# Optimization experiments

Hardware: AMD Instinct MI355X
Metric: run time of the kernel (lower is better)

Reference implementation:

```python
import jax, jax.numpy as jnp
import numpy as np

N = 50000
E = 1600000
IN_FEATS = 256
HIDDEN = 32
HEADS = 4
NUM_CLASSES = 16
NEG_SLOPE = 0.2  # DGL GATConv default leaky_relu slope


def gat_conv(x, src, dst, W, b, attn_l, attn_r, n_nodes):
    """DGL-style GATConv. x:[N,Fin], W:[Fin,H*D], attn_l/attn_r:[H,D], b:[H*D].
    Returns [N, H, D]."""
    H, D = attn_l.shape
    feat = (x @ W).reshape(-1, H, D)                     # [N,H,D]
    el = jnp.sum(feat * attn_l, axis=-1)                 # [N,H]
    er = jnp.sum(feat * attn_r, axis=-1)                 # [N,H]
    e = jax.nn.leaky_relu(el[src] + er[dst], NEG_SLOPE)  # [E,H]
    # segment softmax over incoming edges of each dst node
    m = jax.ops.segment_max(e, dst, num_segments=n_nodes)
    m = jnp.where(jnp.isfinite(m), m, 0.0)               # empty segments -> -inf
    ex = jnp.exp(e - m[dst])                             # [E,H]
    denom = jax.ops.segment_sum(ex, dst, num_segments=n_nodes)
    alpha = ex / jnp.maximum(denom, 1e-9)[dst]           # [E,H]
    msg = feat[src] * alpha[:, :, None]                  # [E,H,D]
    out = jax.ops.segment_sum(msg, dst, num_segments=n_nodes)
    return out + b.reshape(H, D)


def setup_inputs() -> dict:
    key = jax.random.key(0)
    ks = jax.random.split(key, 12)
    x = jax.random.normal(ks[0], (N, IN_FEATS), dtype=jnp.float32)
    src = jax.random.randint(ks[1], (E,), 0, N, dtype=jnp.int32)
    dst = jax.random.randint(ks[2], (E,), 0, N, dtype=jnp.int32)
    s1 = 1.0 / np.sqrt(IN_FEATS)
    W1 = jax.random.normal(ks[3], (IN_FEATS, HEADS * HIDDEN), dtype=jnp.float32) * s1
    b1 = jnp.zeros((HEADS * HIDDEN,), dtype=jnp.float32)
    al1 = jax.random.normal(ks[4], (HEADS, HIDDEN), dtype=jnp.float32) * 0.1
    ar1 = jax.random.normal(ks[5], (HEADS, HIDDEN), dtype=jnp.float32) * 0.1
    F2 = HEADS * HIDDEN
    s2 = 1.0 / np.sqrt(F2)
    W2 = jax.random.normal(ks[6], (F2, NUM_CLASSES), dtype=jnp.float32) * s2
    b2 = jnp.zeros((NUM_CLASSES,), dtype=jnp.float32)
    al2 = jax.random.normal(ks[7], (1, NUM_CLASSES), dtype=jnp.float32) * 0.1
    ar2 = jax.random.normal(ks[8], (1, NUM_CLASSES), dtype=jnp.float32) * 0.1
    return {"x": x, "src": src, "dst": dst,
            "W1": W1, "b1": b1, "al1": al1, "ar1": ar1,
            "W2": W2, "b2": b2, "al2": al2, "ar2": ar2}


def reference(x, src, dst, W1, b1, al1, ar1, W2, b2, al2, ar2):
    h = jax.nn.elu(gat_conv(x, src, dst, W1, b1, al1, ar1, N))  # [N,H,D]
    h = h.reshape(N, HEADS * HIDDEN)                            # flatten(1)
    out = gat_conv(h, src, dst, W2, b2, al2, ar2, N)            # [N,1,C]
    return out.mean(axis=1)                                     # [N,C]
```

## Files before the change

kernel.cpp:

```cpp
#include <hip/hip_runtime.h>
#include <hip/hip_fp16.h>

#define N_NODES 50000
#define N_EDGES 1600000
#define FIN 256
#define HD 128
#define NHEADS 4
#define C2 16
#define NEG 0.2f

#define EBLK 4096
#define NBLK 391
#define NBUCK 391
#define BSH 7
#define BMASK 127
#define MAXB 5120

typedef _Float16 v8h __attribute__((ext_vector_type(8)));
typedef float v4f __attribute__((ext_vector_type(4)));
union F4H8 { float4 f; v8h h; };

__device__ __forceinline__ float elu1(float x) { return x > 0.f ? x : __expf(x) - 1.f; }
__device__ __forceinline__ float lexp(float e) { return __expf(e > 0.f ? e : NEG * e); }


__global__ __launch_bounds__(256) void k_bhist(const int* __restrict__ dst,
                                               int* __restrict__ ghist) {
    __shared__ int lh[NBUCK];
    int tid = threadIdx.x, b = blockIdx.x;
    for (int t = tid; t < NBUCK; t += 256) lh[t] = 0;
    __syncthreads();
    int base = b * EBLK;
    int nq = (min(EBLK, N_EDGES - base)) >> 2;
    const int4* d4 = (const int4*)(dst + base);
    for (int q = tid; q < nq; q += 256) {
        int4 d = d4[q];
        atomicAdd(&lh[d.x >> BSH], 1);
        atomicAdd(&lh[d.y >> BSH], 1);
        atomicAdd(&lh[d.z >> BSH], 1);
        atomicAdd(&lh[d.w >> BSH], 1);
    }
    __syncthreads();
    for (int t = tid; t < NBUCK; t += 256) ghist[t * NBLK + b] = lh[t];
}

__global__ __launch_bounds__(256) void k_bscan1(int* __restrict__ ghist,
                                                int* __restrict__ bucket_tot) {
    __shared__ int s[256];
    int B = blockIdx.x, t = threadIdx.x;
    int* row = ghist + (size_t)B * NBLK;
    int i0 = 2 * t, i1 = 2 * t + 1;
    int a0 = (i0 < NBLK) ? row[i0] : 0;
    int a1 = (i1 < NBLK) ? row[i1] : 0;
    int pair = a0 + a1;
    s[t] = pair;
    __syncthreads();
    for (int off = 1; off < 256; off <<= 1) {
        int u = (t >= off) ? s[t - off] : 0;
        __syncthreads();
        s[t] += u;
        __syncthreads();
    }
    int excl = s[t] - pair;
    if (i0 < NBLK) row[i0] = excl;
    if (i1 < NBLK) row[i1] = excl + a0;
    if (t == 255) bucket_tot[B] = s[255];
}

__global__ __launch_bounds__(512) void k_bscan2(const int* __restrict__ bucket_tot,
                                                int* __restrict__ bucket_base,
                                                int* __restrict__ rowstart) {
    __shared__ int s[512];
    int t = threadIdx.x;
    int v = (t < NBUCK) ? bucket_tot[t] : 0;
    s[t] = v;
    __syncthreads();
    for (int off = 1; off < 512; off <<= 1) {
        int u = (t >= off) ? s[t - off] : 0;
        __syncthreads();
        s[t] += u;
        __syncthreads();
    }
    if (t < NBUCK) bucket_base[t] = s[t] - v;
    if (t == 0) { bucket_base[NBUCK] = N_EDGES; rowstart[N_NODES] = N_EDGES; }
}

__global__ __launch_bounds__(256) void k_bscatter(
        const int* __restrict__ src, const int* __restrict__ dst,
        const int* __restrict__ ghist, const int* __restrict__ bucket_base,
        int* __restrict__ ebuf) {
    __shared__ int lcur[NBUCK];
    int tid = threadIdx.x, b = blockIdx.x;
    for (int t = tid; t < NBUCK; t += 256)
        lcur[t] = bucket_base[t] + ghist[t * NBLK + b];
    __syncthreads();
    int base = b * EBLK;
    int nq = (min(EBLK, N_EDGES - base)) >> 2;
    const int4* s4 = (const int4*)(src + base);
    const int4* d4 = (const int4*)(dst + base);
    for (int q = tid; q < nq; q += 256) {
        int4 s = s4[q];
        int4 d = d4[q];
        int p;
        p = atomicAdd(&lcur[d.x >> BSH], 1); ebuf[p] = (s.x << BSH) | (d.x & BMASK);
        p = atomicAdd(&lcur[d.y >> BSH], 1); ebuf[p] = (s.y << BSH) | (d.y & BMASK);
        p = atomicAdd(&lcur[d.z >> BSH], 1); ebuf[p] = (s.z << BSH) | (d.z & BMASK);
        p = atomicAdd(&lcur[d.w >> BSH], 1); ebuf[p] = (s.w << BSH) | (d.w & BMASK);
    }
}

__global__ __launch_bounds__(256) void k_bsort(
        const int* __restrict__ ebuf, const int* __restrict__ bucket_base,
        int* __restrict__ sorted_src, int* __restrict__ rowstart) {
    __shared__ int ein[MAXB];
    __shared__ int eout[MAXB];
    __shared__ int hist[128];
    __shared__ int sc[128];
    __shared__ int cursor[128];
    int tid = threadIdx.x, B = blockIdx.x;
    int base = bucket_base[B];
    int n = bucket_base[B + 1] - base;
    if (tid < 128) hist[tid] = 0;
    __syncthreads();
    for (int i = tid; i < n; i += 256) {
        int v = ebuf[base + i];
        ein[i] = v;
        atomicAdd(&hist[v & BMASK], 1);
    }
    __syncthreads();
    if (tid < 128) sc[tid] = hist[tid];
    __syncthreads();
    for (int off = 1; off < 128; off <<= 1) {
        int u = 0;
        if (tid < 128 && tid >= off) u = sc[tid - off];
        __syncthreads();
        if (tid < 128) sc[tid] += u;
        __syncthreads();
    }
    if (tid < 128) {
        int ex = sc[tid] - hist[tid];
        cursor[tid] = ex;
        int node = B * 128 + tid;
        if (node < N_NODES) rowstart[node] = base + ex;
    }
    __syncthreads();
    for (int i = tid; i < n; i += 256) {
        int v = ein[i];
        int p = atomicAdd(&cursor[v & BMASK], 1);
        eout[p] = v >> BSH;
    }
    __syncthreads();
    for (int i = tid; i < n; i += 256) sorted_src[base + i] = eout[i];
}


__global__ __launch_bounds__(256) void k_w1half(const float* __restrict__ W1,
                                                _Float16* __restrict__ W1T) {
    int idx = blockIdx.x * 256 + threadIdx.x;
    int k = idx >> 7, c = idx & 127;
    W1T[c * 256 + k] = (_Float16)W1[idx];
}


__global__ __launch_bounds__(256) void k_gemm1(
        const float* __restrict__ x, const _Float16* __restrict__ W1T,
        const float* __restrict__ al1, const float* __restrict__ ar1,
        __half* __restrict__ feat1h, float* __restrict__ el1, float* __restrict__ er1) {
    __shared__ v8h As[64 * 4];
    __shared__ v8h Bs[128 * 4];
    int tid = threadIdx.x;
    int nb = blockIdx.x * 64;
    int wid = tid >> 6, lane = tid & 63;
    int wm = wid & 1, wn = wid >> 1;
    int q = lane >> 4, lm = lane & 15;

    int anode = tid >> 2, ach = tid & 3;
    int gnode = nb + anode; if (gnode >= N_NODES) gnode = N_NODES - 1;
    const float4* xrow = (const float4*)(x + (size_t)gnode * FIN);
    int bc = tid >> 2, bch = tid & 3;

    v4f acc[2][4];
    #pragma unroll
    for (int mt = 0; mt < 2; mt++)
        #pragma unroll
        for (int nt = 0; nt < 4; nt++) acc[mt][nt] = (v4f)(0.f);

    float4 xa0 = xrow[ach * 2];
    float4 xa1 = xrow[ach * 2 + 1];
    F4H8 wb0, wb1;
    wb0.f = *(const float4*)(W1T + bc * 256 + bch * 8);
    wb1.f = *(const float4*)(W1T + (bc + 64) * 256 + bch * 8);

    for (int step = 0; step < 8; step++) {
        __syncthreads();
        {
            v8h av;
            av[0] = (_Float16)xa0.x; av[1] = (_Float16)xa0.y;
            av[2] = (_Float16)xa0.z; av[3] = (_Float16)xa0.w;
            av[4] = (_Float16)xa1.x; av[5] = (_Float16)xa1.y;
            av[6] = (_Float16)xa1.z; av[7] = (_Float16)xa1.w;
            As[anode * 4 + (ach ^ (anode & 3))] = av;
            Bs[bc * 4 + (bch ^ (bc & 3))] = wb0.h;
            Bs[(bc + 64) * 4 + (bch ^ (bc & 3))] = wb1.h;
        }
        __syncthreads();
        if (step < 7) {
            int k0 = (step + 1) * 32;
            xa0 = xrow[(k0 >> 2) + ach * 2];
            xa1 = xrow[(k0 >> 2) + ach * 2 + 1];
            wb0.f = *(const float4*)(W1T + bc * 256 + k0 + bch * 8);
            wb1.f = *(const float4*)(W1T + (bc + 64) * 256 + k0 + bch * 8);
        }
        v8h af[2], bf[4];
        #pragma unroll
        for (int mt = 0; mt < 2; mt++) {
            int nl = wm * 32 + mt * 16 + lm;
            af[mt] = As[nl * 4 + (q ^ (nl & 3))];
        }
        #pragma unroll
        for (int nt = 0; nt < 4; nt++) {
            int cl = wn * 64 + nt * 16 + lm;
            bf[nt] = Bs[cl * 4 + (q ^ (cl & 3))];
        }
        #pragma unroll
        for (int mt = 0; mt < 2; mt++)
            #pragma unroll
            for (int nt = 0; nt < 4; nt++)
                acc[mt][nt] = __builtin_amdgcn_mfma_f32_16x16x32_f16(
                    af[mt], bf[nt], acc[mt][nt], 0, 0, 0);
    }

    float alv[4], arv[4];
    #pragma unroll
    for (int nt = 0; nt < 4; nt++) {
        alv[nt] = al1[wn * 64 + nt * 16 + lm];
        arv[nt] = ar1[wn * 64 + nt * 16 + lm];
    }
    int h0 = 2 * wn, h1 = 2 * wn + 1;
    #pragma unroll
    for (int mt = 0; mt < 2; mt++) {
        #pragma unroll
        for (int r = 0; r < 4; r++) {
            int node = nb + wm * 32 + mt * 16 + q * 4 + r;
            bool ok = node < N_NODES;
            float v0 = acc[mt][0][r], v1 = acc[mt][1][r];
            float v2 = acc[mt][2][r], v3 = acc[mt][3][r];
            if (ok) {
                __half* fp = feat1h + (size_t)node * HD + wn * 64 + lm;
                fp[0]  = __float2half(v0);
                fp[16] = __float2half(v1);
                fp[32] = __float2half(v2);
                fp[48] = __float2half(v3);
            }
            float pl0 = v0 * alv[0] + v1 * alv[1];
            float pr0 = v0 * arv[0] + v1 * arv[1];
            float pl1 = v2 * alv[2] + v3 * alv[3];
            float pr1 = v2 * arv[2] + v3 * arv[3];
            #pragma unroll
            for (int m = 1; m <= 8; m <<= 1) {
                pl0 += __shfl_xor(pl0, m); pr0 += __shfl_xor(pr0, m);
                pl1 += __shfl_xor(pl1, m); pr1 += __shfl_xor(pr1, m);
            }
            if (ok && lm == 0) {
                el1[node * 4 + h0] = pl0; er1[node * 4 + h0] = pr0;
                el1[node * 4 + h1] = pl1; er1[node * 4 + h1] = pr1;
            }
        }
    }
}


__global__ __launch_bounds__(256) void k_agg1(
        const int* __restrict__ rowstart, const int* __restrict__ sorted_src,
        const float* __restrict__ el1, const float* __restrict__ er1,
        const __half* __restrict__ feat1h, const float* __restrict__ b1,
        float* __restrict__ h) {
    int tid = threadIdx.x;
    int d = blockIdx.x * 4 + (tid >> 6);
    int lane = tid & 63;
    int eg = lane >> 4;
    int cl = lane & 15;
    int head = cl >> 2;
    float er = er1[d * 4 + head];
    int start = rowstart[d], end = rowstart[d + 1];
    float acc[8];
    #pragma unroll
    for (int k = 0; k < 8; k++) acc[k] = 0.f;
    float wsum = 0.f;

    for (int i = start; i < end; i += 16) {
        int s[4]; bool ok[4];
        #pragma unroll
        for (int u = 0; u < 4; u++) {
            int e = i + 4 * u + eg;
            ok[u] = e < end;
            int ec = ok[u] ? e : end - 1;
            s[u] = sorted_src[ec];
        }
        float elv[4];
        #pragma unroll
        for (int u = 0; u < 4; u++) elv[u] = el1[s[u] * 4 + head];
        F4H8 r[4];
        #pragma unroll
        for (int u = 0; u < 4; u++)
            r[u].f = *(const float4*)(feat1h + (size_t)s[u] * HD + cl * 8);
        #pragma unroll
        for (int u = 0; u < 4; u++) {
            float w = ok[u] ? lexp(elv[u] + er) : 0.f;
            #pragma unroll
            for (int k = 0; k < 8; k++)
                acc[k] = fmaf((float)r[u].h[k], w, acc[k]);
            wsum += w;
        }
    }
    #pragma unroll
    for (int k = 0; k < 8; k++) {
        acc[k] += __shfl_xor(acc[k], 16);
        acc[k] += __shfl_xor(acc[k], 32);
    }
    wsum += __shfl_xor(wsum, 16);
    wsum += __shfl_xor(wsum, 32);
    if (eg == 0) {
        float inv = 1.f / fmaxf(wsum, 1e-9f);
        float v[8];
        #pragma unroll
        for (int k = 0; k < 8; k++) v[k] = elu1(acc[k] * inv + b1[cl * 8 + k]);
        float4* hp = (float4*)(h + (size_t)d * HD + cl * 8);
        hp[0] = make_float4(v[0], v[1], v[2], v[3]);
        hp[1] = make_float4(v[4], v[5], v[6], v[7]);
    }
}


__global__ __launch_bounds__(256) void k_gemm2(
        const float* __restrict__ h, const float* __restrict__ W2,
        const float* __restrict__ al2, const float* __restrict__ ar2,
        float* __restrict__ feat2, float* __restrict__ el2, float* __restrict__ er2) {
    __shared__ float hs[16 * 132];
    __shared__ float w2t[16 * 132];
    int tid = threadIdx.x;
    int nb = blockIdx.x * 16;
    for (int idx = tid; idx < 512; idx += 256) {
        int row = idx >> 5, kk = idx & 31;
        ((float4*)(hs + row * 132))[kk] = ((const float4*)h)[(size_t)(nb + row) * 32 + kk];
    }
    for (int idx = tid; idx < 2048; idx += 256) {
        int k = idx >> 4, c = idx & 15;
        w2t[c * 132 + k] = W2[idx];
    }
    __syncthreads();
    int nl = tid >> 4, col = tid & 15;
    const float4* hv = (const float4*)(hs + nl * 132);
    const float4* wv = (const float4*)(w2t + col * 132);
    float acc = 0.f;
    #pragma unroll
    for (int kk = 0; kk < 32; kk++) {
        float4 a = hv[kk], w = wv[kk];
        acc += a.x * w.x + a.y * w.y + a.z * w.z + a.w * w.w;
    }
    int node = nb + nl;
    feat2[node * 16 + col] = acc;
    float pl = acc * al2[col], pr = acc * ar2[col];
    #pragma unroll
    for (int m = 8; m >= 1; m >>= 1) {
        pl += __shfl_xor(pl, m);
        pr += __shfl_xor(pr, m);
    }
    if (col == 0) { el2[node] = pl; er2[node] = pr; }
}


__global__ __launch_bounds__(256) void k_agg2(
        const int* __restrict__ rowstart, const int* __restrict__ sorted_src,
        const float* __restrict__ el2, const float* __restrict__ er2,
        const float* __restrict__ feat2, const float* __restrict__ b2,
        float* __restrict__ out) {
    int tid = threadIdx.x;
    int d = blockIdx.x * 4 + (tid >> 6);
    int lane = tid & 63;
    int eg = lane >> 2;
    int cq = lane & 3;
    float er = er2[d];
    int start = rowstart[d], end = rowstart[d + 1];
    float4 acc = make_float4(0.f, 0.f, 0.f, 0.f);
    float wsum = 0.f;
    for (int i = start; i < end; i += 16) {
        int e = i + eg;
        bool ok = e < end;
        int ec = ok ? e : end - 1;
        int s = sorted_src[ec];
        float elv = el2[s];
        float4 f = ((const float4*)feat2)[(size_t)s * 4 + cq];
        float ev = elv + er;
        float wr = __expf(ev > 0.f ? ev : NEG * ev);
        float w = ok ? wr : 0.f;
        acc.x += w * f.x; acc.y += w * f.y; acc.z += w * f.z; acc.w += w * f.w;
        wsum += w;
    }
    #pragma unroll
    for (int m = 4; m <= 32; m <<= 1) {
        acc.x += __shfl_xor(acc.x, m);
        acc.y += __shfl_xor(acc.y, m);
        acc.z += __shfl_xor(acc.z, m);
        acc.w += __shfl_xor(acc.w, m);
        wsum  += __shfl_xor(wsum, m);
    }
    if (lane < 4) {
        float inv = 1.f / fmaxf(wsum, 1e-9f);
        float4 bv = ((const float4*)b2)[cq];
        float4 o = make_float4(acc.x * inv + bv.x, acc.y * inv + bv.y,
                               acc.z * inv + bv.z, acc.w * inv + bv.w);
        ((float4*)out)[(size_t)d * 4 + cq] = o;
    }
}


extern "C" void kernel_launch(void* const* d_in, const int* in_sizes, int n_in,
                              void* d_out, int out_size, void* d_ws, size_t ws_size,
                              hipStream_t stream) {
    const float* x   = (const float*)d_in[0];
    const int*   src = (const int*)d_in[1];
    const int*   dst = (const int*)d_in[2];
    const float* W1  = (const float*)d_in[3];
    const float* b1  = (const float*)d_in[4];
    const float* al1 = (const float*)d_in[5];
    const float* ar1 = (const float*)d_in[6];
    const float* W2  = (const float*)d_in[7];
    const float* b2  = (const float*)d_in[8];
    const float* al2 = (const float*)d_in[9];
    const float* ar2 = (const float*)d_in[10];
    float* out = (float*)d_out;

    char* ws = (char*)d_ws;
    size_t off = 0;
    auto alloc = [&](size_t bytes) -> char* {
        char* p = ws + off;
        off += (bytes + 255) & ~(size_t)255;
        return p;
    };
    __half* feat1h     = (__half*)alloc((size_t)N_NODES * HD * 2);
    _Float16* W1T      = (_Float16*)alloc((size_t)FIN * HD * 2);
    float* h           = (float*)alloc((size_t)N_NODES * HD * 4);
    float* el1         = (float*)alloc((size_t)N_NODES * 4 * 4);
    float* er1         = (float*)alloc((size_t)N_NODES * 4 * 4);
    float* feat2       = (float*)alloc((size_t)N_NODES * C2 * 4);
    float* el2         = (float*)alloc((size_t)N_NODES * 4);
    float* er2         = (float*)alloc((size_t)N_NODES * 4);
    int*   ghist       = (int*)alloc((size_t)NBUCK * NBLK * 4);
    int*   bucket_tot  = (int*)alloc((size_t)NBUCK * 4);
    int*   bucket_base = (int*)alloc((size_t)(NBUCK + 1) * 4);
    int*   rowstart    = (int*)alloc((size_t)(N_NODES + 1) * 4);
    int*   ebuf        = (int*)alloc((size_t)N_EDGES * 4);
    int*   sorted_src  = (int*)alloc((size_t)N_EDGES * 4);

    k_bhist<<<NBLK, 256, 0, stream>>>(dst, ghist);
    k_bscan1<<<NBUCK, 256, 0, stream>>>(ghist, bucket_tot);
    k_bscan2<<<1, 512, 0, stream>>>(bucket_tot, bucket_base, rowstart);
    k_bscatter<<<NBLK, 256, 0, stream>>>(src, dst, ghist, bucket_base, ebuf);
    k_bsort<<<NBUCK, 256, 0, stream>>>(ebuf, bucket_base, sorted_src, rowstart);
    k_w1half<<<128, 256, 0, stream>>>(W1, W1T);
    k_gemm1<<<(N_NODES + 63) / 64, 256, 0, stream>>>(x, W1T, al1, ar1, feat1h, el1, er1);
    k_agg1<<<N_NODES / 4, 256, 0, stream>>>(rowstart, sorted_src, el1, er1, feat1h, b1, h);
    k_gemm2<<<N_NODES / 16, 256, 0, stream>>>(h, W2, al2, ar2, feat2, el2, er2);
    k_agg2<<<N_NODES / 4, 256, 0, stream>>>(rowstart, sorted_src, el2, er2, feat2, b2, out);
}
```

Measured before the change: 246.6 us.

## Merge independent graph-sort and GEMM stages into shared launches; widen agg2 edge parallelism

Independent work is co-scheduled inside single launches. The bucket histogram now shares a kernel with the W1 fp16 transpose, and the edge scatter shares one with the first-layer GEMM. This cuts two kernel launches and lets the memory-bound scatter overlap with GEMM compute. The layer-2 aggregation now assigns 32 edges per wave iteration, with each lane handling 8 channels instead of 4, which halves loop trips but adds more registers and shuffles. The merged kernel uses a shared-memory union sized for the GEMM, and the heterogeneous blocks may cause load imbalance.

```diff
diff --git a/kernel.cpp b/kernel.cpp
--- a/kernel.cpp
+++ b/kernel.cpp
@@ -24,24 +24,33 @@
 __device__ __forceinline__ float lexp(float e) { return __expf(e > 0.f ? e : NEG * e); }
 
 
-__global__ __launch_bounds__(256) void k_bhist(const int* __restrict__ dst,
-                                               int* __restrict__ ghist) {
+__global__ __launch_bounds__(256) void k_front(const int* __restrict__ dst,
+                                               int* __restrict__ ghist,
+                                               const float* __restrict__ W1,
+                                               _Float16* __restrict__ W1T) {
     __shared__ int lh[NBUCK];
-    int tid = threadIdx.x, b = blockIdx.x;
-    for (int t = tid; t < NBUCK; t += 256) lh[t] = 0;
-    __syncthreads();
-    int base = b * EBLK;
-    int nq = (min(EBLK, N_EDGES - base)) >> 2;
-    const int4* d4 = (const int4*)(dst + base);
-    for (int q = tid; q < nq; q += 256) {
-        int4 d = d4[q];
-        atomicAdd(&lh[d.x >> BSH], 1);
-        atomicAdd(&lh[d.y >> BSH], 1);
-        atomicAdd(&lh[d.z >> BSH], 1);
-        atomicAdd(&lh[d.w >> BSH], 1);
-    }
-    __syncthreads();
-    for (int t = tid; t < NBUCK; t += 256) ghist[t * NBLK + b] = lh[t];
+    int tid = threadIdx.x;
+    if (blockIdx.x < NBLK) {
+        int b = blockIdx.x;
+        for (int t = tid; t < NBUCK; t += 256) lh[t] = 0;
+        __syncthreads();
+        int base = b * EBLK;
+        int nq = (min(EBLK, N_EDGES - base)) >> 2;
+        const int4* d4 = (const int4*)(dst + base);
+        for (int q = tid; q < nq; q += 256) {
+            int4 d = d4[q];
+            atomicAdd(&lh[d.x >> BSH], 1);
+            atomicAdd(&lh[d.y >> BSH], 1);
+            atomicAdd(&lh[d.z >> BSH], 1);
+            atomicAdd(&lh[d.w >> BSH], 1);
+        }
+        __syncthreads();
+        for (int t = tid; t < NBUCK; t += 256) ghist[t * NBLK + b] = lh[t];
+    } else {
+        int idx = (blockIdx.x - NBLK) * 256 + tid;
+        int k = idx >> 7, c = idx & 127;
+        W1T[c * 256 + k] = (_Float16)W1[idx];
+    }
 }
 
 __global__ __launch_bounds__(256) void k_bscan1(int* __restrict__ ghist,
@@ -85,91 +94,40 @@
     if (t == 0) { bucket_base[NBUCK] = N_EDGES; rowstart[N_NODES] = N_EDGES; }
 }
 
-__global__ __launch_bounds__(256) void k_bscatter(
+
+__global__ __launch_bounds__(256) void k_mid(
         const int* __restrict__ src, const int* __restrict__ dst,
         const int* __restrict__ ghist, const int* __restrict__ bucket_base,
-        int* __restrict__ ebuf) {
-    __shared__ int lcur[NBUCK];
-    int tid = threadIdx.x, b = blockIdx.x;
-    for (int t = tid; t < NBUCK; t += 256)
-        lcur[t] = bucket_base[t] + ghist[t * NBLK + b];
-    __syncthreads();
-    int base = b * EBLK;
-    int nq = (min(EBLK, N_EDGES - base)) >> 2;
-    const int4* s4 = (const int4*)(src + base);
-    const int4* d4 = (const int4*)(dst + base);
-    for (int q = tid; q < nq; q += 256) {
-        int4 s = s4[q];
-        int4 d = d4[q];
-        int p;
-        p = atomicAdd(&lcur[d.x >> BSH], 1); ebuf[p] = (s.x << BSH) | (d.x & BMASK);
-        p = atomicAdd(&lcur[d.y >> BSH], 1); ebuf[p] = (s.y << BSH) | (d.y & BMASK);
-        p = atomicAdd(&lcur[d.z >> BSH], 1); ebuf[p] = (s.z << BSH) | (d.z & BMASK);
-        p = atomicAdd(&lcur[d.w >> BSH], 1); ebuf[p] = (s.w << BSH) | (d.w & BMASK);
-    }
-}
-
-__global__ __launch_bounds__(256) void k_bsort(
-        const int* __restrict__ ebuf, const int* __restrict__ bucket_base,
-        int* __restrict__ sorted_src, int* __restrict__ rowstart) {
-    __shared__ int ein[MAXB];
-    __shared__ int eout[MAXB];
-    __shared__ int hist[128];
-    __shared__ int sc[128];
-    __shared__ int cursor[128];
-    int tid = threadIdx.x, B = blockIdx.x;
-    int base = bucket_base[B];
-    int n = bucket_base[B + 1] - base;
-    if (tid < 128) hist[tid] = 0;
-    __syncthreads();
-    for (int i = tid; i < n; i += 256) {
-        int v = ebuf[base + i];
-        ein[i] = v;
-        atomicAdd(&hist[v & BMASK], 1);
-    }
-    __syncthreads();
-    if (tid < 128) sc[tid] = hist[tid];
-    __syncthreads();
-    for (int off = 1; off < 128; off <<= 1) {
-        int u = 0;
-        if (tid < 128 && tid >= off) u = sc[tid - off];
-        __syncthreads();
-        if (tid < 128) sc[tid] += u;
-        __syncthreads();
-    }
-    if (tid < 128) {
-        int ex = sc[tid] - hist[tid];
-        cursor[tid] = ex;
-        int node = B * 128 + tid;
-        if (node < N_NODES) rowstart[node] = base + ex;
-    }
-    __syncthreads();
-    for (int i = tid; i < n; i += 256) {
-        int v = ein[i];
-        int p = atomicAdd(&cursor[v & BMASK], 1);
-        eout[p] = v >> BSH;
-    }
-    __syncthreads();
-    for (int i = tid; i < n; i += 256) sorted_src[base + i] = eout[i];
-}
-
-
-__global__ __launch_bounds__(256) void k_w1half(const float* __restrict__ W1,
-                                                _Float16* __restrict__ W1T) {
-    int idx = blockIdx.x * 256 + threadIdx.x;
-    int k = idx >> 7, c = idx & 127;
-    W1T[c * 256 + k] = (_Float16)W1[idx];
-}
-
-
-__global__ __launch_bounds__(256) void k_gemm1(
+        int* __restrict__ ebuf,
         const float* __restrict__ x, const _Float16* __restrict__ W1T,
         const float* __restrict__ al1, const float* __restrict__ ar1,
         __half* __restrict__ feat1h, float* __restrict__ el1, float* __restrict__ er1) {
-    __shared__ v8h As[64 * 4];
-    __shared__ v8h Bs[128 * 4];
+    __shared__ __align__(16) char smem[12288];
     int tid = threadIdx.x;
-    int nb = blockIdx.x * 64;
+    if (blockIdx.x < NBLK) {
+        int* lcur = (int*)smem;
+        int b = blockIdx.x;
+        for (int t = tid; t < NBUCK; t += 256)
+            lcur[t] = bucket_base[t] + ghist[t * NBLK + b];
+        __syncthreads();
+        int base = b * EBLK;
+        int nq = (min(EBLK, N_EDGES - base)) >> 2;
+        const int4* s4 = (const int4*)(src + base);
+        const int4* d4 = (const int4*)(dst + base);
+        for (int q = tid; q < nq; q += 256) {
+            int4 s = s4[q];
+            int4 d = d4[q];
+            int p;
+            p = atomicAdd(&lcur[d.x >> BSH], 1); ebuf[p] = (s.x << BSH) | (d.x & BMASK);
+            p = atomicAdd(&lcur[d.y >> BSH], 1); ebuf[p] = (s.y << BSH) | (d.y & BMASK);
+            p = atomicAdd(&lcur[d.z >> BSH], 1); ebuf[p] = (s.z << BSH) | (d.z & BMASK);
+            p = atomicAdd(&lcur[d.w >> BSH], 1); ebuf[p] = (s.w << BSH) | (d.w & BMASK);
+        }
+        return;
+    }
+    v8h* As = (v8h*)smem;
+    v8h* Bs = (v8h*)(smem + 4096);
+    int nb = (blockIdx.x - NBLK) * 64;
     int wid = tid >> 6, lane = tid & 63;
     int wm = wid & 1, wn = wid >> 1;
     int q = lane >> 4, lm = lane & 15;
@@ -269,6 +227,50 @@
     }
 }
 
+__global__ __launch_bounds__(256) void k_bsort(
+        const int* __restrict__ ebuf, const int* __restrict__ bucket_base,
+        int* __restrict__ sorted_src, int* __restrict__ rowstart) {
+    __shared__ int ein[MAXB];
+    __shared__ int eout[MAXB];
+    __shared__ int hist[128];
+    __shared__ int sc[128];
+    __shared__ int cursor[128];
+    int tid = threadIdx.x, B = blockIdx.x;
+    int base = bucket_base[B];
+    int n = bucket_base[B + 1] - base;
+    if (tid < 128) hist[tid] = 0;
+    __syncthreads();
+    for (int i = tid; i < n; i += 256) {
+        int v = ebuf[base + i];
+        ein[i] = v;
+        atomicAdd(&hist[v & BMASK], 1);
+    }
+    __syncthreads();
+    if (tid < 128) sc[tid] = hist[tid];
+    __syncthreads();
+    for (int off = 1; off < 128; off <<= 1) {
+        int u = 0;
+        if (tid < 128 && tid >= off) u = sc[tid - off];
+        __syncthreads();
+        if (tid < 128) sc[tid] += u;
+        __syncthreads();
+    }
+    if (tid < 128) {
+        int ex = sc[tid] - hist[tid];
+        cursor[tid] = ex;
+        int node = B * 128 + tid;
+        if (node < N_NODES) rowstart[node] = base + ex;
+    }
+    __syncthreads();
+    for (int i = tid; i < n; i += 256) {
+        int v = ein[i];
+        int p = atomicAdd(&cursor[v & BMASK], 1);
+        eout[p] = v >> BSH;
+    }
+    __syncthreads();
+    for (int i = tid; i < n; i += 256) sorted_src[base + i] = eout[i];
+}
+
 
 __global__ __launch_bounds__(256) void k_agg1(
         const int* __restrict__ rowstart, const int* __restrict__ sorted_src,
@@ -378,39 +380,43 @@
     int tid = threadIdx.x;
     int d = blockIdx.x * 4 + (tid >> 6);
     int lane = tid & 63;
-    int eg = lane >> 2;
-    int cq = lane & 3;
+    int eg = lane >> 1;
+    int half = lane & 1;
     float er = er2[d];
     int start = rowstart[d], end = rowstart[d + 1];
-    float4 acc = make_float4(0.f, 0.f, 0.f, 0.f);
+    float acc[8];
+    #pragma unroll
+    for (int k = 0; k < 8; k++) acc[k] = 0.f;
     float wsum = 0.f;
-    for (int i = start; i < end; i += 16) {
+    const float4* f4 = (const float4*)feat2;
+    for (int i = start; i < end; i += 32) {
         int e = i + eg;
         bool ok = e < end;
         int ec = ok ? e : end - 1;
         int s = sorted_src[ec];
         float elv = el2[s];
-        float4 f = ((const float4*)feat2)[(size_t)s * 4 + cq];
-        float ev = elv + er;
-        float wr = __expf(ev > 0.f ? ev : NEG * ev);
-        float w = ok ? wr : 0.f;
-        acc.x += w * f.x; acc.y += w * f.y; acc.z += w * f.z; acc.w += w * f.w;
+        float4 f0 = f4[(size_t)s * 4 + half * 2];
+        float4 f1 = f4[(size_t)s * 4 + half * 2 + 1];
+        float w = ok ? lexp(elv + er) : 0.f;
+        acc[0] += w * f0.x; acc[1] += w * f0.y; acc[2] += w * f0.z; acc[3] += w * f0.w;
+        acc[4] += w * f1.x; acc[5] += w * f1.y; acc[6] += w * f1.z; acc[7] += w * f1.w;
         wsum += w;
     }
     #pragma unroll
-    for (int m = 4; m <= 32; m <<= 1) {
-        acc.x += __shfl_xor(acc.x, m);
-        acc.y += __shfl_xor(acc.y, m);
-        acc.z += __shfl_xor(acc.z, m);
-        acc.w += __shfl_xor(acc.w, m);
-        wsum  += __shfl_xor(wsum, m);
-    }
-    if (lane < 4) {
+    for (int m = 2; m <= 32; m <<= 1) {
+        #pragma unroll
+        for (int k = 0; k < 8; k++) acc[k] += __shfl_xor(acc[k], m);
+        wsum += __shfl_xor(wsum, m);
+    }
+    if (eg == 0) {
         float inv = 1.f / fmaxf(wsum, 1e-9f);
-        float4 bv = ((const float4*)b2)[cq];
-        float4 o = make_float4(acc.x * inv + bv.x, acc.y * inv + bv.y,
-                               acc.z * inv + bv.z, acc.w * inv + bv.w);
-        ((float4*)out)[(size_t)d * 4 + cq] = o;
+        float4 b0 = ((const float4*)b2)[half * 2];
+        float4 b1 = ((const float4*)b2)[half * 2 + 1];
+        float4* op = (float4*)out + (size_t)d * 4 + half * 2;
+        op[0] = make_float4(acc[0] * inv + b0.x, acc[1] * inv + b0.y,
+                            acc[2] * inv + b0.z, acc[3] * inv + b0.w);
+        op[1] = make_float4(acc[4] * inv + b1.x, acc[5] * inv + b1.y,
+                            acc[6] * inv + b1.z, acc[7] * inv + b1.w);
     }
 }
 
@@ -453,13 +459,12 @@
     int*   ebuf        = (int*)alloc((size_t)N_EDGES * 4);
     int*   sorted_src  = (int*)alloc((size_t)N_EDGES * 4);
 
-    k_bhist<<<NBLK, 256, 0, stream>>>(dst, ghist);
+    k_front<<<NBLK + 128, 256, 0, stream>>>(dst, ghist, W1, W1T);
     k_bscan1<<<NBUCK, 256, 0, stream>>>(ghist, bucket_tot);
     k_bscan2<<<1, 512, 0, stream>>>(bucket_tot, bucket_base, rowstart);
-    k_bscatter<<<NBLK, 256, 0, stream>>>(src, dst, ghist, bucket_base, ebuf);
+    k_mid<<<NBLK + 782, 256, 0, stream>>>(src, dst, ghist, bucket_base, ebuf,
+                                          x, W1T, al1, ar1, feat1h, el1, er1);
     k_bsort<<<NBUCK, 256, 0, stream>>>(ebuf, bucket_base, sorted_src, rowstart);
-    k_w1half<<<128, 256, 0, stream>>>(W1, W1T);
-    k_gemm1<<<(N_NODES + 63) / 64, 256, 0, stream>>>(x, W1T, al1, ar1, feat1h, el1, er1);
     k_agg1<<<N_NODES / 4, 256, 0, stream>>>(rowstart, sorted_src, el1, er1, feat1h, b1, h);
     k_gemm2<<<N_NODES / 16, 256, 0, stream>>>(h, W2, al2, ar2, feat2, el2, er2);
     k_agg2<<<N_NODES / 4, 256, 0, stream>>>(rowstart, sorted_src, el2, er2, feat2, b2, out);
```

Result: no change. 251.3 us (+1.9%).
